# Performance work log

Hardware: AMD Instinct MI355X
Metric: run time of the kernel (lower is better)

The kernel has to match this reference:

```python
import jax, jax.numpy as jnp
import numpy as np

NUM_NODES = 100000
NUM_EDGES = 50000
NUM_CONN = 800000
IN_DIM = 256
HIDDEN = 128
EDGE_ATTR_DIM = 17
LN_EPS = 1e-5


def setup_inputs() -> dict:
    key = jax.random.key(0)
    k1, k2, k3, kw1, kb1, kg, kbeta, kw2, kb2 = jax.random.split(key, 9)
    node_features = jax.random.normal(k1, (NUM_NODES, IN_DIM), dtype=jnp.float32)
    nodes = jax.random.randint(k2, (NUM_CONN,), 0, NUM_NODES, dtype=jnp.int64)
    edges = jax.random.randint(k3, (NUM_CONN,), 0, NUM_EDGES, dtype=jnp.int64)
    hyperedge_index = jnp.stack([nodes, edges], axis=0)
    # MLP params (Linear(in,hid) -> LayerNorm -> ReLU -> Dropout(eval:identity) -> Linear(hid,out))
    W1 = jax.random.normal(kw1, (IN_DIM, HIDDEN), dtype=jnp.float32) * (1.0 / np.sqrt(IN_DIM))
    b1 = jax.random.normal(kb1, (HIDDEN,), dtype=jnp.float32) * 0.01
    ln_g = jnp.ones((HIDDEN,), dtype=jnp.float32)
    ln_b = jnp.zeros((HIDDEN,), dtype=jnp.float32)
    W2 = jax.random.normal(kw2, (HIDDEN, EDGE_ATTR_DIM), dtype=jnp.float32) * (1.0 / np.sqrt(HIDDEN))
    b2 = jax.random.normal(kb2, (EDGE_ATTR_DIM,), dtype=jnp.float32) * 0.01
    return {"node_features": node_features, "hyperedge_index": hyperedge_index,
            "W1": W1, "b1": b1, "ln_g": ln_g, "ln_b": ln_b, "W2": W2, "b2": b2}


def reference(node_features, hyperedge_index, W1, b1, ln_g, ln_b, W2, b2):
    nodes = hyperedge_index[0]
    edges = hyperedge_index[1]
    # indices are in-range by construction (torch valid_mask is all-True here)
    gathered = node_features[nodes]                         # [num_conn, in_dim]
    summed = jax.ops.segment_sum(gathered, edges, num_segments=NUM_EDGES)
    counts = jax.ops.segment_sum(jnp.ones(edges.shape, node_features.dtype), edges,
                                 num_segments=NUM_EDGES)
    edge_features = summed / jnp.clip(counts, 1.0)[:, None]  # mean aggregation
    # decoder MLP (dropout inactive in eval)
    h = edge_features @ W1 + b1
    mu = jnp.mean(h, axis=-1, keepdims=True)
    var = jnp.mean(jnp.square(h - mu), axis=-1, keepdims=True)
    h = (h - mu) * jax.lax.rsqrt(var + LN_EPS) * ln_g + ln_b
    h = jax.nn.relu(h)
    return h @ W2 + b2                                      # [num_edges, edge_attr_dim]
```

## Files before the change

kernel.cpp:

```cpp
#include <hip/hip_runtime.h>
#include <hip/hip_bf16.h>
#include <stdint.h>

#define NUM_NODES 100000
#define NUM_EDGES 50000
#define NUM_CONN  800000
#define IN_DIM    256
#define HIDDEN    128
#define EDGE_DIM  17
#define PAD       64

typedef __bf16 bf16x8 __attribute__((ext_vector_type(8)));
typedef float  f32x4  __attribute__((ext_vector_type(4)));


__global__ void prep_kernel(const float* __restrict__ W1, const float* __restrict__ W2,
                            __bf16* __restrict__ w1f, __bf16* __restrict__ w2f,
                            int* __restrict__ counts) {
    int i = blockIdx.x * 256 + threadIdx.x;
    if (i < NUM_EDGES) counts[i] = 0;
    if (i < 4096) {
        int lane = i & 63, t = (i >> 6) & 7, kc2 = i >> 9;
        int m = lane & 15, q = lane >> 4;
        int n = t * 16 + m;
        int kbase = kc2 * 32 + q * 8;
        __bf16* dst = w1f + (size_t)i * 8;
        #pragma unroll
        for (int ki = 0; ki < 8; ++ki)
            dst[ki] = (__bf16)W1[(size_t)(kbase + ki) * HIDDEN + n];
    } else if (i < 4608) {
        int f = i - 4096;
        int lane = f & 63, t = (f >> 6) & 1, ks = f >> 7;
        int m = lane & 15, q = lane >> 4;
        int n = t * 16 + m;
        int kbase = ks * 32 + q * 8;
        __bf16* dst = w2f + (size_t)f * 8;
        #pragma unroll
        for (int ki = 0; ki < 8; ++ki)
            dst[ki] = (n < EDGE_DIM) ? (__bf16)W2[(size_t)(kbase + ki) * EDGE_DIM + n]
                                     : (__bf16)0.0f;
    }
}

__global__ void bucket_kernel(const int* __restrict__ idx,
                              int* __restrict__ counts, int* __restrict__ slots) {
    int i = blockIdx.x * 256 + threadIdx.x;
    if (i >= NUM_CONN / 2) return;
    int4 vn = ((const int4*)idx)[i];
    int4 ve = ((const int4*)(idx + 2 * NUM_CONN))[i];
    int p0 = atomicAdd(&counts[ve.x], 1);
    if (p0 < PAD) slots[(size_t)ve.x * PAD + p0] = vn.x;
    int p1 = atomicAdd(&counts[ve.z], 1);
    if (p1 < PAD) slots[(size_t)ve.z * PAD + p1] = vn.z;
}

__global__ void bucket_kernel_i32(const int* __restrict__ idx,
                                  int* __restrict__ counts, int* __restrict__ slots) {
    int i = blockIdx.x * 256 + threadIdx.x;
    if (i >= NUM_CONN) return;
    int node = idx[i];
    int edge = idx[NUM_CONN + i];
    int pos = atomicAdd(&counts[edge], 1);
    if (pos < PAD) slots[(size_t)edge * PAD + pos] = node;
}

__global__ __launch_bounds__(256) void proj_kernel(const float* __restrict__ nf,
                                                   const __bf16* __restrict__ w1f,
                                                   __bf16* __restrict__ pbf) {
    const int wave = threadIdx.x >> 6;
    const int lane = threadIdx.x & 63;
    const int m = lane & 15, q = lane >> 4;
    const int rowbase = blockIdx.x * 128 + wave * 32;
    const bf16x8* __restrict__ frag = (const bf16x8*)w1f;

    f32x4 acc[2][8];
    #pragma unroll
    for (int mt = 0; mt < 2; ++mt)
        #pragma unroll
        for (int t = 0; t < 8; ++t) acc[mt][t] = (f32x4){0.f, 0.f, 0.f, 0.f};

    const float* ap[2];
    #pragma unroll
    for (int mt = 0; mt < 2; ++mt) {
        int r = rowbase + mt * 16 + m;
        if (r >= NUM_NODES) r = NUM_NODES - 1;
        ap[mt] = nf + (size_t)r * IN_DIM + q * 8;
    }

    #pragma unroll
    for (int kc2 = 0; kc2 < 8; ++kc2) {
        bf16x8 b[8];
        #pragma unroll
        for (int t = 0; t < 8; ++t) b[t] = frag[(kc2 * 8 + t) * 64 + lane];
        #pragma unroll
        for (int mt = 0; mt < 2; ++mt) {
            float4 f0 = *(const float4*)(ap[mt] + kc2 * 32);
            float4 f1 = *(const float4*)(ap[mt] + kc2 * 32 + 4);
            bf16x8 a;
            a[0] = (__bf16)f0.x; a[1] = (__bf16)f0.y;
            a[2] = (__bf16)f0.z; a[3] = (__bf16)f0.w;
            a[4] = (__bf16)f1.x; a[5] = (__bf16)f1.y;
            a[6] = (__bf16)f1.z; a[7] = (__bf16)f1.w;
            #pragma unroll
            for (int t = 0; t < 8; ++t)
                acc[mt][t] = __builtin_amdgcn_mfma_f32_16x16x32_bf16(a, b[t], acc[mt][t], 0, 0, 0);
        }
    }

    #pragma unroll
    for (int mt = 0; mt < 2; ++mt) {
        int ob = rowbase + mt * 16 + q * 4;
        #pragma unroll
        for (int t = 0; t < 8; ++t)
            #pragma unroll
            for (int r = 0; r < 4; ++r) {
                int orow = ob + r;
                if (orow < NUM_NODES)
                    pbf[(size_t)orow * HIDDEN + t * 16 + m] = (__bf16)acc[mt][t][r];
            }
    }
}

__global__ __launch_bounds__(256) void edge_kernel(const uint4* __restrict__ p4,
        const int* __restrict__ counts, const int* __restrict__ slots,
        const float* __restrict__ b1, const float* __restrict__ ln_g,
        const float* __restrict__ ln_b, uint4* __restrict__ rws) {
    const int wave = threadIdx.x >> 6;
    const int lane = threadIdx.x & 63;
    const int g = lane & 15, ge = lane >> 4;
    const int e = blockIdx.x * 16 + wave * 4 + ge;

    const int c = counts[e];
    const int cc = c < PAD ? c : PAD;
    const float inv = 1.0f / (float)(c > 0 ? c : 1);

    float acc[8];
    #pragma unroll
    for (int d = 0; d < 8; ++d) acc[d] = 0.f;

    for (int c0 = 0; c0 < cc; c0 += 16) {
        int slv = slots[(size_t)e * PAD + c0 + g];
        int lim = cc - c0; if (lim > 16) lim = 16;
        if (lim == 16) {
            #pragma unroll
            for (int k0 = 0; k0 < 16; k0 += 4) {
                uint4 u[4];
                #pragma unroll
                for (int k = 0; k < 4; ++k) {
                    int nd = __shfl(slv, ge * 16 + k0 + k, 64);
                    u[k] = p4[(size_t)nd * 16 + g];
                }
                #pragma unroll
                for (int k = 0; k < 4; ++k) {
                    acc[0] += __uint_as_float(u[k].x << 16);
                    acc[1] += __uint_as_float(u[k].x & 0xffff0000u);
                    acc[2] += __uint_as_float(u[k].y << 16);
                    acc[3] += __uint_as_float(u[k].y & 0xffff0000u);
                    acc[4] += __uint_as_float(u[k].z << 16);
                    acc[5] += __uint_as_float(u[k].z & 0xffff0000u);
                    acc[6] += __uint_as_float(u[k].w << 16);
                    acc[7] += __uint_as_float(u[k].w & 0xffff0000u);
                }
            }
        } else {
            for (int k0 = 0; k0 < lim; k0 += 4) {
                uint4 u[4];
                unsigned okm[4];
                #pragma unroll
                for (int k = 0; k < 4; ++k) {
                    int nd = __shfl(slv, ge * 16 + k0 + k, 64);
                    nd = ((unsigned)nd < NUM_NODES) ? nd : 0;
                    u[k] = p4[(size_t)nd * 16 + g];
                    okm[k] = (k0 + k < lim) ? 0xffffffffu : 0u;
                }
                #pragma unroll
                for (int k = 0; k < 4; ++k) {
                    uint4 v = u[k];
                    v.x &= okm[k]; v.y &= okm[k]; v.z &= okm[k]; v.w &= okm[k];
                    acc[0] += __uint_as_float(v.x << 16);
                    acc[1] += __uint_as_float(v.x & 0xffff0000u);
                    acc[2] += __uint_as_float(v.y << 16);
                    acc[3] += __uint_as_float(v.y & 0xffff0000u);
                    acc[4] += __uint_as_float(v.z << 16);
                    acc[5] += __uint_as_float(v.z & 0xffff0000u);
                    acc[6] += __uint_as_float(v.w << 16);
                    acc[7] += __uint_as_float(v.w & 0xffff0000u);
                }
            }
        }
    }

    float4 bA = ((const float4*)b1)[2 * g];
    float4 bB = ((const float4*)b1)[2 * g + 1];
    float h[8];
    h[0] = acc[0] * inv + bA.x; h[1] = acc[1] * inv + bA.y;
    h[2] = acc[2] * inv + bA.z; h[3] = acc[3] * inv + bA.w;
    h[4] = acc[4] * inv + bB.x; h[5] = acc[5] * inv + bB.y;
    h[6] = acc[6] * inv + bB.z; h[7] = acc[7] * inv + bB.w;

    float s = 0.f;
    #pragma unroll
    for (int d = 0; d < 8; ++d) s += h[d];
    #pragma unroll
    for (int off = 8; off > 0; off >>= 1) s += __shfl_xor(s, off, 64);
    float mu = s * (1.0f / 128.0f);

    float dv[8], vv = 0.f;
    #pragma unroll
    for (int d = 0; d < 8; ++d) { dv[d] = h[d] - mu; vv += dv[d] * dv[d]; }
    #pragma unroll
    for (int off = 8; off > 0; off >>= 1) vv += __shfl_xor(vv, off, 64);
    float rs = rsqrtf(vv * (1.0f / 128.0f) + 1e-5f);

    float4 gA = ((const float4*)ln_g)[2 * g];
    float4 gB = ((const float4*)ln_g)[2 * g + 1];
    float4 eA = ((const float4*)ln_b)[2 * g];
    float4 eB = ((const float4*)ln_b)[2 * g + 1];
    float gg[8] = {gA.x, gA.y, gA.z, gA.w, gB.x, gB.y, gB.z, gB.w};
    float ee[8] = {eA.x, eA.y, eA.z, eA.w, eB.x, eB.y, eB.z, eB.w};
    union { __bf16 b[8]; uint4 u; } pk;
    #pragma unroll
    for (int d = 0; d < 8; ++d) {
        float r = dv[d] * rs * gg[d] + ee[d];
        pk.b[d] = (__bf16)(r > 0.f ? r : 0.f);
    }
    rws[(size_t)e * 16 + g] = pk.u;
}

__global__ __launch_bounds__(256) void out_kernel(const __bf16* __restrict__ rws,
        const __bf16* __restrict__ w2f, const float* __restrict__ b2,
        float* __restrict__ out) {
    __shared__ __align__(16) __bf16 lds[4096];
    {
        const uint4* s = (const uint4*)w2f;
        uint4* d = (uint4*)lds;
        #pragma unroll
        for (int i = threadIdx.x; i < 512; i += 256) d[i] = s[i];
    }
    __syncthreads();
    const int wave = threadIdx.x >> 6;
    const int lane = threadIdx.x & 63;
    const int tile = blockIdx.x * 4 + wave;
    if (tile >= NUM_EDGES / 16) return;
    const int m = lane & 15, q = lane >> 4;
    const bf16x8* frag = (const bf16x8*)lds;
    const __bf16* arow = rws + ((size_t)tile * 16 + m) * HIDDEN + q * 8;

    f32x4 acc0 = (f32x4){0.f, 0.f, 0.f, 0.f};
    f32x4 acc1 = (f32x4){0.f, 0.f, 0.f, 0.f};
    #pragma unroll
    for (int s = 0; s < 4; ++s) {
        bf16x8 a = *(const bf16x8*)(arow + s * 32);
        acc0 = __builtin_amdgcn_mfma_f32_16x16x32_bf16(a, frag[(s * 2 + 0) * 64 + lane], acc0, 0, 0, 0);
        acc1 = __builtin_amdgcn_mfma_f32_16x16x32_bf16(a, frag[(s * 2 + 1) * 64 + lane], acc1, 0, 0, 0);
    }
    int rowb = tile * 16 + q * 4;
    float bm = b2[m];
    #pragma unroll
    for (int r = 0; r < 4; ++r) {
        out[(size_t)(rowb + r) * EDGE_DIM + m] = acc0[r] + bm;
        if (m == 0) out[(size_t)(rowb + r) * EDGE_DIM + 16] = acc1[r] + b2[16];
    }
}

extern "C" void kernel_launch(void* const* d_in, const int* in_sizes, int n_in,
                              void* d_out, int out_size, void* d_ws, size_t ws_size,
                              hipStream_t stream) {
    const float* nf  = (const float*)d_in[0];
    const int*   idx = (const int*)d_in[1];
    const float* W1  = (const float*)d_in[2];
    const float* b1  = (const float*)d_in[3];
    const float* g   = (const float*)d_in[4];
    const float* be  = (const float*)d_in[5];
    const float* W2  = (const float*)d_in[6];
    const float* b2  = (const float*)d_in[7];
    float* out = (float*)d_out;

    char* ws = (char*)d_ws;
    __bf16* P      = (__bf16*)ws;
    int*    counts = (int*)(ws + 25600000);
    int*    slots  = (int*)(ws + 25800000);
    __bf16* W1F    = (__bf16*)(ws + 38600000);
    __bf16* W2F    = (__bf16*)(ws + 38665536);
    __bf16* R      = (__bf16*)(ws + 38673728);

    int stride = (in_sizes[1] == 2 * NUM_CONN) ? 1 : 2;

    prep_kernel<<<196, 256, 0, stream>>>(W1, W2, W1F, W2F, counts);
    if (stride == 2)
        bucket_kernel<<<(NUM_CONN / 2 + 255) / 256, 256, 0, stream>>>(idx, counts, slots);
    else
        bucket_kernel_i32<<<(NUM_CONN + 255) / 256, 256, 0, stream>>>(idx, counts, slots);
    proj_kernel<<<(NUM_NODES + 127) / 128, 256, 0, stream>>>(nf, W1F, P);
    edge_kernel<<<NUM_EDGES / 16, 256, 0, stream>>>((const uint4*)P, counts, slots,
                                                    b1, g, be, (uint4*)R);
    out_kernel<<<(NUM_EDGES / 16 + 3) / 4, 256, 0, stream>>>(R, W2F, b2, out);
}
```

Before: 275.6 us.

## Fuse bucketing with projection and fold output GEMM into edge kernel

Bucketing and node projection now run in one launch: two of every three blocks bucket connections and the third runs projection tiles, so the atomic-heavy scatter can overlap with the MFMA projection. The output Linear is moved into the edge kernel, which stages the 16 normalized hidden rows in LDS and has wave 0 run the small MFMA. This drops the intermediate R buffer round trip and two kernel launches. The int64 index path is removed, so the code now assumes int32 indices.

Result: faster. 252.7 us (-8.3%).

```diff
diff --git a/kernel.cpp b/kernel.cpp
--- a/kernel.cpp
+++ b/kernel.cpp
@@ -42,35 +42,29 @@
     }
 }
 
-__global__ void bucket_kernel(const int* __restrict__ idx,
-                              int* __restrict__ counts, int* __restrict__ slots) {
-    int i = blockIdx.x * 256 + threadIdx.x;
-    if (i >= NUM_CONN / 2) return;
-    int4 vn = ((const int4*)idx)[i];
-    int4 ve = ((const int4*)(idx + 2 * NUM_CONN))[i];
-    int p0 = atomicAdd(&counts[ve.x], 1);
-    if (p0 < PAD) slots[(size_t)ve.x * PAD + p0] = vn.x;
-    int p1 = atomicAdd(&counts[ve.z], 1);
-    if (p1 < PAD) slots[(size_t)ve.z * PAD + p1] = vn.z;
-}
-
-__global__ void bucket_kernel_i32(const int* __restrict__ idx,
-                                  int* __restrict__ counts, int* __restrict__ slots) {
-    int i = blockIdx.x * 256 + threadIdx.x;
-    if (i >= NUM_CONN) return;
-    int node = idx[i];
-    int edge = idx[NUM_CONN + i];
-    int pos = atomicAdd(&counts[edge], 1);
-    if (pos < PAD) slots[(size_t)edge * PAD + pos] = node;
-}
-
-__global__ __launch_bounds__(256) void proj_kernel(const float* __restrict__ nf,
-                                                   const __bf16* __restrict__ w1f,
-                                                   __bf16* __restrict__ pbf) {
+#define FRONT_BLOCKS 2346
+__global__ __launch_bounds__(256) void front_kernel(const int* __restrict__ idx,
+        int* __restrict__ counts, int* __restrict__ slots,
+        const float* __restrict__ nf, const __bf16* __restrict__ w1f,
+        __bf16* __restrict__ pbf) {
+    if (blockIdx.x % 3 != 2) {
+        int b = blockIdx.x - blockIdx.x / 3;
+        int i = b * 256 + threadIdx.x;
+        if (i < NUM_CONN / 2) {
+            int2 vn = ((const int2*)idx)[i];
+            int2 ve = ((const int2*)(idx + NUM_CONN))[i];
+            int p0 = atomicAdd(&counts[ve.x], 1);
+            if (p0 < PAD) slots[(size_t)ve.x * PAD + p0] = vn.x;
+            int p1 = atomicAdd(&counts[ve.y], 1);
+            if (p1 < PAD) slots[(size_t)ve.y * PAD + p1] = vn.y;
+        }
+        return;
+    }
+    const int p_idx = blockIdx.x / 3;
     const int wave = threadIdx.x >> 6;
     const int lane = threadIdx.x & 63;
     const int m = lane & 15, q = lane >> 4;
-    const int rowbase = blockIdx.x * 128 + wave * 32;
+    const int rowbase = p_idx * 128 + wave * 32;
     const bf16x8* __restrict__ frag = (const bf16x8*)w1f;
 
     f32x4 acc[2][8];
@@ -124,11 +118,14 @@
 __global__ __launch_bounds__(256) void edge_kernel(const uint4* __restrict__ p4,
         const int* __restrict__ counts, const int* __restrict__ slots,
         const float* __restrict__ b1, const float* __restrict__ ln_g,
-        const float* __restrict__ ln_b, uint4* __restrict__ rws) {
+        const float* __restrict__ ln_b, const __bf16* __restrict__ w2f,
+        const float* __restrict__ b2, float* __restrict__ out) {
+    __shared__ __align__(16) uint4 lds_r[256];
     const int wave = threadIdx.x >> 6;
     const int lane = threadIdx.x & 63;
     const int g = lane & 15, ge = lane >> 4;
-    const int e = blockIdx.x * 16 + wave * 4 + ge;
+    const int el = wave * 4 + ge;
+    const int e = blockIdx.x * 16 + el;
 
     const int c = counts[e];
     const int cc = c < PAD ? c : PAD;
@@ -224,42 +221,29 @@
         float r = dv[d] * rs * gg[d] + ee[d];
         pk.b[d] = (__bf16)(r > 0.f ? r : 0.f);
     }
-    rws[(size_t)e * 16 + g] = pk.u;
-}
-
-__global__ __launch_bounds__(256) void out_kernel(const __bf16* __restrict__ rws,
-        const __bf16* __restrict__ w2f, const float* __restrict__ b2,
-        float* __restrict__ out) {
-    __shared__ __align__(16) __bf16 lds[4096];
-    {
-        const uint4* s = (const uint4*)w2f;
-        uint4* d = (uint4*)lds;
-        #pragma unroll
-        for (int i = threadIdx.x; i < 512; i += 256) d[i] = s[i];
-    }
+    lds_r[el * 16 + g] = pk.u;
     __syncthreads();
-    const int wave = threadIdx.x >> 6;
-    const int lane = threadIdx.x & 63;
-    const int tile = blockIdx.x * 4 + wave;
-    if (tile >= NUM_EDGES / 16) return;
-    const int m = lane & 15, q = lane >> 4;
-    const bf16x8* frag = (const bf16x8*)lds;
-    const __bf16* arow = rws + ((size_t)tile * 16 + m) * HIDDEN + q * 8;
-
-    f32x4 acc0 = (f32x4){0.f, 0.f, 0.f, 0.f};
-    f32x4 acc1 = (f32x4){0.f, 0.f, 0.f, 0.f};
-    #pragma unroll
-    for (int s = 0; s < 4; ++s) {
-        bf16x8 a = *(const bf16x8*)(arow + s * 32);
-        acc0 = __builtin_amdgcn_mfma_f32_16x16x32_bf16(a, frag[(s * 2 + 0) * 64 + lane], acc0, 0, 0, 0);
-        acc1 = __builtin_amdgcn_mfma_f32_16x16x32_bf16(a, frag[(s * 2 + 1) * 64 + lane], acc1, 0, 0, 0);
-    }
-    int rowb = tile * 16 + q * 4;
-    float bm = b2[m];
-    #pragma unroll
-    for (int r = 0; r < 4; ++r) {
-        out[(size_t)(rowb + r) * EDGE_DIM + m] = acc0[r] + bm;
-        if (m == 0) out[(size_t)(rowb + r) * EDGE_DIM + 16] = acc1[r] + b2[16];
+
+    if (wave == 0) {
+        const int m = lane & 15, q = lane >> 4;
+        const __bf16* lr = (const __bf16*)lds_r;
+        const bf16x8* fw = (const bf16x8*)w2f;
+        f32x4 a0 = (f32x4){0.f, 0.f, 0.f, 0.f};
+        f32x4 a1 = (f32x4){0.f, 0.f, 0.f, 0.f};
+        #pragma unroll
+        for (int ks = 0; ks < 4; ++ks) {
+            bf16x8 a = *(const bf16x8*)(lr + m * 128 + ks * 32 + q * 8);
+            a0 = __builtin_amdgcn_mfma_f32_16x16x32_bf16(a, fw[(ks * 2 + 0) * 64 + lane], a0, 0, 0, 0);
+            a1 = __builtin_amdgcn_mfma_f32_16x16x32_bf16(a, fw[(ks * 2 + 1) * 64 + lane], a1, 0, 0, 0);
+        }
+        int rowb = blockIdx.x * 16 + q * 4;
+        float bm = b2[m];
+        float b16 = b2[16];
+        #pragma unroll
+        for (int r = 0; r < 4; ++r) {
+            out[(size_t)(rowb + r) * EDGE_DIM + m] = a0[r] + bm;
+            if (m == 0) out[(size_t)(rowb + r) * EDGE_DIM + 16] = a1[r] + b16;
+        }
     }
 }
 
@@ -282,17 +266,9 @@
     int*    slots  = (int*)(ws + 25800000);
     __bf16* W1F    = (__bf16*)(ws + 38600000);
     __bf16* W2F    = (__bf16*)(ws + 38665536);
-    __bf16* R      = (__bf16*)(ws + 38673728);
-
-    int stride = (in_sizes[1] == 2 * NUM_CONN) ? 1 : 2;
 
     prep_kernel<<<196, 256, 0, stream>>>(W1, W2, W1F, W2F, counts);
-    if (stride == 2)
-        bucket_kernel<<<(NUM_CONN / 2 + 255) / 256, 256, 0, stream>>>(idx, counts, slots);
-    else
-        bucket_kernel_i32<<<(NUM_CONN + 255) / 256, 256, 0, stream>>>(idx, counts, slots);
-    proj_kernel<<<(NUM_NODES + 127) / 128, 256, 0, stream>>>(nf, W1F, P);
+    front_kernel<<<FRONT_BLOCKS, 256, 0, stream>>>(idx, counts, slots, nf, W1F, P);
     edge_kernel<<<NUM_EDGES / 16, 256, 0, stream>>>((const uint4*)P, counts, slots,
-                                                    b1, g, be, (uint4*)R);
-    out_kernel<<<(NUM_EDGES / 16 + 3) / 4, 256, 0, stream>>>(R, W2F, b2, out);
-}
+                                                    b1, g, be, W2F, b2, out);
+}
```
